# Optimization experiments

Hardware: AMD Instinct MI355X
Metric: run time of the kernel (lower is better)

## Reference

```python
import jax, jax.numpy as jnp
import numpy as np

N_NODES = 100000
N_EDGES = 1600000
IN_FEAT = 128
UNITS = 64


def setup_inputs() -> dict:
    key = jax.random.key(0)
    k1, k2, k3, k4, k5 = jax.random.split(key, 5)
    node_states = jax.random.normal(k1, (N_NODES, IN_FEAT), dtype=jnp.float32)
    # edges[:,0] is the destination/segment id; the original TF code's
    # repeat(bincount) normalization assumes edges sorted by edges[:,0].
    dst = jnp.sort(jax.random.randint(k2, (N_EDGES,), 0, N_NODES))
    src = jax.random.randint(k3, (N_EDGES,), 0, N_NODES)
    edges = jnp.stack([dst, src], axis=1).astype(jnp.int64)
    kernel = jax.random.normal(k4, (IN_FEAT, UNITS), dtype=jnp.float32) * 0.05
    kernel_attention = jax.random.normal(k5, (2 * UNITS, 1), dtype=jnp.float32) * 0.05
    return {"node_states": node_states, "edges": edges,
            "kernel": kernel, "kernel_attention": kernel_attention}


def reference(node_states, edges, kernel, kernel_attention):
    n_nodes = node_states.shape[0]
    dst = edges[:, 0]  # segment ids (aggregation target)
    src = edges[:, 1]  # neighbor being gathered

    h = node_states @ kernel                      # [N, U]
    h_dst = h[dst]                                # [E, U]
    h_src = h[src]                                # [E, U]
    # concat(h_dst, h_src) @ a  ==  h_dst @ a[:U] + h_src @ a[U:]
    u = kernel_attention.shape[0] // 2
    scores = (h_dst @ kernel_attention[:u] + h_src @ kernel_attention[u:])[:, 0]  # [E]
    scores = jax.nn.leaky_relu(scores, negative_slope=0.2)  # tf default alpha=0.2
    scores = jnp.exp(jnp.clip(scores, -2.0, 2.0))

    score_sum = jax.ops.segment_sum(scores, dst, num_segments=n_nodes)  # [N]
    attn = scores / score_sum[dst]                                      # [E]

    out = jax.ops.segment_sum(h_src * attn[:, None], dst, num_segments=n_nodes)  # [N, U]
    return out
```

## Files before the change

### kernel.cpp

```cpp
#include <hip/hip_runtime.h>
#include <hip/hip_bf16.h>

#define NN 100000
#define NE 1600000
#define NF 128
#define UU 64

typedef __attribute__((ext_vector_type(8))) short short8;
typedef __attribute__((ext_vector_type(4))) float f32x4;

static const size_t OFF_FLAG = 0;
static const size_t OFF_EW   = 256;
static const size_t OFF_H2   = OFF_EW  + (size_t)NE * 8;
static const size_t OFF_AD   = OFF_H2  + (size_t)NN * UU * 2;
static const size_t OFF_AS   = OFF_AD  + (size_t)NN * 4;
static const size_t OFF_ROW  = OFF_AS  + (size_t)NN * 4;
static const size_t OFF_WP   = OFF_ROW + (size_t)(NN + 1) * 4;

__device__ __forceinline__ unsigned short bfr(float v) {
    unsigned u = __float_as_uint(v);
    return (unsigned short)((u + 0x7FFFu + ((u >> 16) & 1u)) >> 16);
}

__global__ __launch_bounds__(256) void prep(const int* __restrict__ ew,
                                            const float* __restrict__ W,
                                            int* __restrict__ flag,
                                            unsigned short* __restrict__ Wp) {
    if (blockIdx.x == 0) {
        if (threadIdx.x == 0) {
            int a = ew[2 * 400000 + 1] | ew[2 * 800000 + 1] |
                    ew[2 * 1200000 + 1] | ew[2 * 1599999 + 1];
            *flag = (a == 0) ? 1 : 0;
        }
        return;
    }
    int i = (blockIdx.x - 1) * 256 + threadIdx.x;
    int j   = i & 7;
    int l15 = (i >> 3) & 15;
    int quad = (i >> 7) & 3;
    int kb  = (i >> 9) & 3;
    int nt  = i >> 11;
    Wp[i] = bfr(W[(size_t)(kb * 32 + quad * 8 + j) * UU + nt * 16 + l15]);
}

#define GEMM_BLOCKS   1563
#define ROWS_BLOCKS   391

__global__ __launch_bounds__(256) void mega(const float* __restrict__ X,
                                            const void* __restrict__ edges,
                                            const int* __restrict__ flag,
                                            const unsigned short* __restrict__ Wp,
                                            const float* __restrict__ ka,
                                            unsigned short* __restrict__ h2,
                                            float* __restrict__ a_dst,
                                            float* __restrict__ a_src,
                                            int* __restrict__ rows) {
    int bid = blockIdx.x;
    int tid = threadIdx.x;

    if (bid < GEMM_BLOCKS) {
        int wv = tid >> 6, lane = tid & 63;
        int quad = lane >> 4, l15 = lane & 15;
        int nb = bid * 64 + wv * 16;
        int row = nb + l15; if (row >= NN) row = NN - 1;
        const float* xr = X + (size_t)row * NF + quad * 8;

        short8 afrag[4];
#pragma unroll
        for (int kb = 0; kb < 4; kb++) {
            float4 p0 = *(const float4*)(xr + kb * 32);
            float4 p1 = *(const float4*)(xr + kb * 32 + 4);
            short8 a;
            a[0] = (short)bfr(p0.x); a[1] = (short)bfr(p0.y);
            a[2] = (short)bfr(p0.z); a[3] = (short)bfr(p0.w);
            a[4] = (short)bfr(p1.x); a[5] = (short)bfr(p1.y);
            a[6] = (short)bfr(p1.z); a[7] = (short)bfr(p1.w);
            afrag[kb] = a;
        }

        f32x4 acc[4] = {f32x4{0,0,0,0}, f32x4{0,0,0,0}, f32x4{0,0,0,0}, f32x4{0,0,0,0}};
        const short8* wpf = (const short8*)Wp;
#pragma unroll
        for (int nt = 0; nt < 4; nt++) {
#pragma unroll
            for (int kb = 0; kb < 4; kb++) {
                short8 b = wpf[((nt * 4 + kb) * 4 + quad) * 16 + l15];
                acc[nt] = __builtin_amdgcn_mfma_f32_16x16x32_bf16(afrag[kb], b, acc[nt], 0, 0, 0);
            }
        }

        float kad[4], kas[4];
#pragma unroll
        for (int nt = 0; nt < 4; nt++) {
            kad[nt] = ka[nt * 16 + l15];
            kas[nt] = ka[64 + nt * 16 + l15];
        }
#pragma unroll
        for (int r = 0; r < 4; r++) {
            int m = nb + quad * 4 + r;
            if (m < NN) {
#pragma unroll
                for (int nt = 0; nt < 4; nt++)
                    h2[(size_t)m * UU + nt * 16 + l15] = bfr(acc[nt][r]);
            }
            float pd = acc[0][r] * kad[0] + acc[1][r] * kad[1] + acc[2][r] * kad[2] + acc[3][r] * kad[3];
            float ps = acc[0][r] * kas[0] + acc[1][r] * kas[1] + acc[2][r] * kas[2] + acc[3][r] * kas[3];
            pd += __shfl_xor(pd, 1); pd += __shfl_xor(pd, 2);
            pd += __shfl_xor(pd, 4); pd += __shfl_xor(pd, 8);
            ps += __shfl_xor(ps, 1); ps += __shfl_xor(ps, 2);
            ps += __shfl_xor(ps, 4); ps += __shfl_xor(ps, 8);
            if (l15 == 0 && m < NN) { a_dst[m] = pd; a_src[m] = ps; }
        }
        return;
    }
    bid -= GEMM_BLOCKS;

    {
        int n = bid * 256 + tid;
        if (n > NN) return;
        if (n == NN) { rows[NN] = NE; return; }
        int fl = *flag;
        const int* ew = (const int*)edges;
        int lo = 0, hi = NE;
        while (lo < hi) {
            int mid = (lo + hi) >> 1;
            int d = fl ? ew[4 * (size_t)mid] : ew[2 * (size_t)mid];
            if (d < n) lo = mid + 1; else hi = mid;
        }
        rows[n] = lo;
    }
}

__device__ __forceinline__ float edge_score(float ad, float as) {
    float sc = ad + as;
    sc = sc > 0.f ? sc : 0.2f * sc;
    sc = fminf(fmaxf(sc, -2.f), 2.f);
    return __expf(sc);
}

__global__ __launch_bounds__(256) void wkern(const void* __restrict__ edges,
                                             const int* __restrict__ flag,
                                             const float* __restrict__ a_dst,
                                             const float* __restrict__ a_src,
                                             int2* __restrict__ ew8) {
    int fl = *flag;
    int tid = threadIdx.x;
    if (fl) {
        const int4* ev = (const int4*)edges;
#pragma unroll
        for (int t = 0; t < 4; t++) {
            int i = blockIdx.x * 1024 + t * 256 + tid;
            if (i < NE) {
                int4 v = ev[i];
                float w = edge_score(a_dst[v.x], a_src[v.z]);
                ew8[i] = make_int2(v.z, __float_as_int(w));
            }
        }
    } else {
        const int4* ev = (const int4*)edges;
#pragma unroll
        for (int t = 0; t < 2; t++) {
            int p = blockIdx.x * 512 + t * 256 + tid;
            if (p * 2 < NE) {
                int4 v = ev[p];
                float w0 = edge_score(a_dst[v.x], a_src[v.y]);
                float w1 = edge_score(a_dst[v.z], a_src[v.w]);
                int4 o = make_int4(v.y, __float_as_int(w0), v.w, __float_as_int(w1));
                *(int4*)(ew8 + p * 2) = o;
            }
        }
    }
}

__global__ __launch_bounds__(256) void aggregate(const int* __restrict__ rows,
                                                 const int2* __restrict__ ew8,
                                                 const unsigned short* __restrict__ h2,
                                                 float* __restrict__ out) {
    int gid = blockIdx.x * blockDim.x + threadIdx.x;
    int n = gid >> 6;
    int lane = gid & 63;
    if (n >= NN) return;
    int s = rows[n], e = rows[n + 1];
    int cnt = e - s;
    int g = lane >> 4, gl = lane & 15;
    const unsigned short* h2g = h2 + gl * 4;
    float4 acc = make_float4(0.f, 0.f, 0.f, 0.f);

#define GBATCH(C0, N)                                                            \
    {                                                                            \
        uint2 rr[4]; float sw[4]; int sjv[4];                                    \
        _Pragma("unroll")                                                        \
        for (int t = 0; t < (N); t++) {                                          \
            int j = (C0) + t * 4 + g;                                            \
            sjv[t] = __shfl(mysrc, j);                                           \
            sw[t]  = __shfl(myw, j);                                             \
        }                                                                        \
        _Pragma("unroll")                                                        \
        for (int t = 0; t < (N); t++)                                            \
            rr[t] = *(const uint2*)(h2g + (size_t)sjv[t] * UU);                  \
        _Pragma("unroll")                                                        \
        for (int t = 0; t < (N); t++) {                                          \
            acc.x += sw[t] * __uint_as_float(rr[t].x << 16);                     \
            acc.y += sw[t] * __uint_as_float(rr[t].x & 0xFFFF0000u);             \
            acc.z += sw[t] * __uint_as_float(rr[t].y << 16);                     \
            acc.w += sw[t] * __uint_as_float(rr[t].y & 0xFFFF0000u);             \
        }                                                                        \
    }

    float inv;
    if (cnt <= 64) {
        int idx = s + lane;
        int mysrc = 0; float myw = 0.f;
        if (idx < e) { int2 p = ew8[idx]; mysrc = p.x; myw = __int_as_float(p.y); }
        int c = 0;
        for (; c + 16 <= cnt; c += 16) GBATCH(c, 4);
        int rem = cnt - c;
        if (rem > 12)     GBATCH(c, 4)
        else if (rem > 8) GBATCH(c, 3)
        else if (rem > 4) GBATCH(c, 2)
        else if (rem > 0) GBATCH(c, 1);
        float t = myw;
#pragma unroll
        for (int off = 32; off; off >>= 1) t += __shfl_xor(t, off);
        inv = (cnt > 0) ? 1.f / t : 0.f;
    } else {
        float ssum = 0.f;
        for (int i = s + lane; i < e; i += 64) ssum += __int_as_float(ew8[i].y);
#pragma unroll
        for (int off = 32; off; off >>= 1) ssum += __shfl_xor(ssum, off);
        inv = 1.f / ssum;
        for (int c0 = s; c0 < e; c0 += 64) {
            int i = c0 + lane;
            int mysrc = 0; float myw = 0.f;
            if (i < e) { int2 p = ew8[i]; mysrc = p.x; myw = __int_as_float(p.y); }
            GBATCH(0, 4); GBATCH(16, 4); GBATCH(32, 4); GBATCH(48, 4);
        }
    }
#undef GBATCH

    acc.x += __shfl_xor(acc.x, 32); acc.y += __shfl_xor(acc.y, 32);
    acc.z += __shfl_xor(acc.z, 32); acc.w += __shfl_xor(acc.w, 32);
    acc.x += __shfl_xor(acc.x, 16); acc.y += __shfl_xor(acc.y, 16);
    acc.z += __shfl_xor(acc.z, 16); acc.w += __shfl_xor(acc.w, 16);
    if (lane < 16) {
        float4 o = make_float4(acc.x * inv, acc.y * inv, acc.z * inv, acc.w * inv);
        *(float4*)(out + (size_t)n * UU + gl * 4) = o;
    }
}

extern "C" void kernel_launch(void* const* d_in, const int* in_sizes, int n_in,
                              void* d_out, int out_size, void* d_ws, size_t ws_size,
                              hipStream_t stream) {
    const float* X  = (const float*)d_in[0];
    const void*  Ed = d_in[1];
    const float* W  = (const float*)d_in[2];
    const float* KA = (const float*)d_in[3];
    float* out = (float*)d_out;

    char* ws = (char*)d_ws;
    int*            flag  = (int*)(ws + OFF_FLAG);
    int2*           ew8   = (int2*)(ws + OFF_EW);
    unsigned short* h2    = (unsigned short*)(ws + OFF_H2);
    float*          a_dst = (float*)(ws + OFF_AD);
    float*          a_src = (float*)(ws + OFF_AS);
    int*            rows  = (int*)(ws + OFF_ROW);
    unsigned short* Wp    = (unsigned short*)(ws + OFF_WP);

    prep<<<33, 256, 0, stream>>>((const int*)Ed, W, flag, Wp);
    mega<<<GEMM_BLOCKS + ROWS_BLOCKS, 256, 0, stream>>>(
        X, Ed, flag, Wp, KA, h2, a_dst, a_src, rows);
    wkern<<<1563, 256, 0, stream>>>(Ed, flag, a_dst, a_src, ew8);
    aggregate<<<(NN * 64 + 255) / 256, 256, 0, stream>>>(rows, ew8, h2, out);
}
```

Measured before the change: 162.4 us.

## Fuse edge-score kernel into aggregation, one node per 16-lane group

Removes the separate wkern pass that wrote (src, weight) pairs to a workspace buffer. Attention scores are now computed inside the aggregation kernel straight from the edge array and a_src. Each wave now handles four nodes, one per 16-lane group, instead of one node per wave, which cuts idle lanes at an average degree of about 16. The cost is strided 8- or 16-byte reads of the int64 edge array, scattered a_src gathers inside the aggregate kernel, and more divergence when node degrees differ within a wave.

New measurement: 145.2 us. 10.6% less time.

```diff
diff --git a/kernel.cpp b/kernel.cpp
--- a/kernel.cpp
+++ b/kernel.cpp
@@ -10,8 +10,7 @@
 typedef __attribute__((ext_vector_type(4))) float f32x4;
 
 static const size_t OFF_FLAG = 0;
-static const size_t OFF_EW   = 256;
-static const size_t OFF_H2   = OFF_EW  + (size_t)NE * 8;
+static const size_t OFF_H2   = 256;
 static const size_t OFF_AD   = OFF_H2  + (size_t)NN * UU * 2;
 static const size_t OFF_AS   = OFF_AD  + (size_t)NN * 4;
 static const size_t OFF_ROW  = OFF_AS  + (size_t)NN * 4;
@@ -138,114 +137,101 @@
     return __expf(sc);
 }
 
-__global__ __launch_bounds__(256) void wkern(const void* __restrict__ edges,
-                                             const int* __restrict__ flag,
-                                             const float* __restrict__ a_dst,
-                                             const float* __restrict__ a_src,
-                                             int2* __restrict__ ew8) {
-    int fl = *flag;
-    int tid = threadIdx.x;
-    if (fl) {
-        const int4* ev = (const int4*)edges;
-#pragma unroll
-        for (int t = 0; t < 4; t++) {
-            int i = blockIdx.x * 1024 + t * 256 + tid;
-            if (i < NE) {
-                int4 v = ev[i];
-                float w = edge_score(a_dst[v.x], a_src[v.z]);
-                ew8[i] = make_int2(v.z, __float_as_int(w));
-            }
-        }
-    } else {
-        const int4* ev = (const int4*)edges;
-#pragma unroll
-        for (int t = 0; t < 2; t++) {
-            int p = blockIdx.x * 512 + t * 256 + tid;
-            if (p * 2 < NE) {
-                int4 v = ev[p];
-                float w0 = edge_score(a_dst[v.x], a_src[v.y]);
-                float w1 = edge_score(a_dst[v.z], a_src[v.w]);
-                int4 o = make_int4(v.y, __float_as_int(w0), v.w, __float_as_int(w1));
-                *(int4*)(ew8 + p * 2) = o;
-            }
-        }
-    }
-}
-
-__global__ __launch_bounds__(256) void aggregate(const int* __restrict__ rows,
-                                                 const int2* __restrict__ ew8,
+__global__ __launch_bounds__(256) void aggregate(const void* __restrict__ edges,
+                                                 const int* __restrict__ flag,
+                                                 const int* __restrict__ rows,
+                                                 const float* __restrict__ a_dst,
+                                                 const float* __restrict__ a_src,
                                                  const unsigned short* __restrict__ h2,
                                                  float* __restrict__ out) {
-    int gid = blockIdx.x * blockDim.x + threadIdx.x;
-    int n = gid >> 6;
-    int lane = gid & 63;
+    int tid = threadIdx.x;
+    int lane = tid & 63;
+    int g = lane >> 4, gl = lane & 15;
+    int n = blockIdx.x * 16 + (tid >> 6) * 4 + g;
     if (n >= NN) return;
     int s = rows[n], e = rows[n + 1];
     int cnt = e - s;
-    int g = lane >> 4, gl = lane & 15;
+    float ad = a_dst[n];
+    int fl = *flag;
+    const int* ew = (const int*)edges;
+    const int* sp = ew + (fl ? 2 : 1);
+    int lsh = fl ? 2 : 1;
     const unsigned short* h2g = h2 + gl * 4;
+    int gbase = g * 16;
     float4 acc = make_float4(0.f, 0.f, 0.f, 0.f);
-
-#define GBATCH(C0, N)                                                            \
-    {                                                                            \
-        uint2 rr[4]; float sw[4]; int sjv[4];                                    \
-        _Pragma("unroll")                                                        \
-        for (int t = 0; t < (N); t++) {                                          \
-            int j = (C0) + t * 4 + g;                                            \
-            sjv[t] = __shfl(mysrc, j);                                           \
-            sw[t]  = __shfl(myw, j);                                             \
-        }                                                                        \
-        _Pragma("unroll")                                                        \
-        for (int t = 0; t < (N); t++)                                            \
-            rr[t] = *(const uint2*)(h2g + (size_t)sjv[t] * UU);                  \
-        _Pragma("unroll")                                                        \
-        for (int t = 0; t < (N); t++) {                                          \
-            acc.x += sw[t] * __uint_as_float(rr[t].x << 16);                     \
-            acc.y += sw[t] * __uint_as_float(rr[t].x & 0xFFFF0000u);             \
-            acc.z += sw[t] * __uint_as_float(rr[t].y << 16);                     \
-            acc.w += sw[t] * __uint_as_float(rr[t].y & 0xFFFF0000u);             \
-        }                                                                        \
-    }
-
     float inv;
+
+#define BATCH(MS, MW, BOFF)                                                  \
+    {                                                                        \
+        uint2 rr[4]; float sw[4]; int sjv[4];                                \
+        _Pragma("unroll")                                                    \
+        for (int t = 0; t < 4; t++) {                                        \
+            sjv[t] = __shfl(MS, gbase + (BOFF) + t);                         \
+            sw[t]  = __shfl(MW, gbase + (BOFF) + t);                         \
+        }                                                                    \
+        _Pragma("unroll")                                                    \
+        for (int t = 0; t < 4; t++)                                          \
+            rr[t] = *(const uint2*)(h2g + (size_t)sjv[t] * UU);              \
+        _Pragma("unroll")                                                    \
+        for (int t = 0; t < 4; t++) {                                        \
+            acc.x += sw[t] * __uint_as_float(rr[t].x << 16);                 \
+            acc.y += sw[t] * __uint_as_float(rr[t].x & 0xFFFF0000u);         \
+            acc.z += sw[t] * __uint_as_float(rr[t].y << 16);                 \
+            acc.w += sw[t] * __uint_as_float(rr[t].y & 0xFFFF0000u);         \
+        }                                                                    \
+    }
+
     if (cnt <= 64) {
-        int idx = s + lane;
-        int mysrc = 0; float myw = 0.f;
-        if (idx < e) { int2 p = ew8[idx]; mysrc = p.x; myw = __int_as_float(p.y); }
-        int c = 0;
-        for (; c + 16 <= cnt; c += 16) GBATCH(c, 4);
-        int rem = cnt - c;
-        if (rem > 12)     GBATCH(c, 4)
-        else if (rem > 8) GBATCH(c, 3)
-        else if (rem > 4) GBATCH(c, 2)
-        else if (rem > 0) GBATCH(c, 1);
-        float t = myw;
-#pragma unroll
-        for (int off = 32; off; off >>= 1) t += __shfl_xor(t, off);
-        inv = (cnt > 0) ? 1.f / t : 0.f;
+        int msrc[4]; float mw[4];
+#pragma unroll
+        for (int k = 0; k < 4; k++) {
+            int c = k * 16 + gl;
+            int sj = 0; float w = 0.f;
+            if (c < cnt) {
+                sj = sp[(size_t)(s + c) << lsh];
+                w = edge_score(ad, a_src[sj]);
+            }
+            msrc[k] = sj; mw[k] = w;
+        }
+        float t0 = (mw[0] + mw[1]) + (mw[2] + mw[3]);
+        t0 += __shfl_xor(t0, 1); t0 += __shfl_xor(t0, 2);
+        t0 += __shfl_xor(t0, 4); t0 += __shfl_xor(t0, 8);
+        inv = (cnt > 0) ? 1.f / t0 : 0.f;
+#pragma unroll
+        for (int k = 0; k < 4; k++) {
+#pragma unroll
+            for (int b = 0; b < 4; b++) {
+                if (k * 16 + b * 4 < cnt) BATCH(msrc[k], mw[k], b * 4);
+            }
+        }
     } else {
-        float ssum = 0.f;
-        for (int i = s + lane; i < e; i += 64) ssum += __int_as_float(ew8[i].y);
-#pragma unroll
-        for (int off = 32; off; off >>= 1) ssum += __shfl_xor(ssum, off);
-        inv = 1.f / ssum;
-        for (int c0 = s; c0 < e; c0 += 64) {
-            int i = c0 + lane;
-            int mysrc = 0; float myw = 0.f;
-            if (i < e) { int2 p = ew8[i]; mysrc = p.x; myw = __int_as_float(p.y); }
-            GBATCH(0, 4); GBATCH(16, 4); GBATCH(32, 4); GBATCH(48, 4);
-        }
-    }
-#undef GBATCH
-
-    acc.x += __shfl_xor(acc.x, 32); acc.y += __shfl_xor(acc.y, 32);
-    acc.z += __shfl_xor(acc.z, 32); acc.w += __shfl_xor(acc.w, 32);
-    acc.x += __shfl_xor(acc.x, 16); acc.y += __shfl_xor(acc.y, 16);
-    acc.z += __shfl_xor(acc.z, 16); acc.w += __shfl_xor(acc.w, 16);
-    if (lane < 16) {
-        float4 o = make_float4(acc.x * inv, acc.y * inv, acc.z * inv, acc.w * inv);
-        *(float4*)(out + (size_t)n * UU + gl * 4) = o;
-    }
+        float t0 = 0.f;
+        for (int c = gl; c < cnt; c += 16) {
+            int sj = sp[(size_t)(s + c) << lsh];
+            t0 += edge_score(ad, a_src[sj]);
+        }
+        t0 += __shfl_xor(t0, 1); t0 += __shfl_xor(t0, 2);
+        t0 += __shfl_xor(t0, 4); t0 += __shfl_xor(t0, 8);
+        inv = 1.f / t0;
+        for (int c0 = 0; c0 < cnt; c0 += 16) {
+            int c = c0 + gl;
+            int sj = 0; float w = 0.f;
+            if (c < cnt) {
+                sj = sp[(size_t)(s + c) << lsh];
+                w = edge_score(ad, a_src[sj]);
+            }
+#pragma unroll
+            for (int b = 0; b < 4; b++) {
+                if (c0 + b * 4 < cnt) BATCH(sj, w, b * 4);
+            }
+        }
+    }
+#undef BATCH
+
+    float4 o;
+    o.x = acc.x * inv; o.y = acc.y * inv;
+    o.z = acc.z * inv; o.w = acc.w * inv;
+    *(float4*)(out + (size_t)n * UU + gl * 4) = o;
 }
 
 extern "C" void kernel_launch(void* const* d_in, const int* in_sizes, int n_in,
@@ -259,7 +245,6 @@
 
     char* ws = (char*)d_ws;
     int*            flag  = (int*)(ws + OFF_FLAG);
-    int2*           ew8   = (int2*)(ws + OFF_EW);
     unsigned short* h2    = (unsigned short*)(ws + OFF_H2);
     float*          a_dst = (float*)(ws + OFF_AD);
     float*          a_src = (float*)(ws + OFF_AS);
@@ -269,6 +254,5 @@
     prep<<<33, 256, 0, stream>>>((const int*)Ed, W, flag, Wp);
     mega<<<GEMM_BLOCKS + ROWS_BLOCKS, 256, 0, stream>>>(
         X, Ed, flag, Wp, KA, h2, a_dst, a_src, rows);
-    wkern<<<1563, 256, 0, stream>>>(Ed, flag, a_dst, a_src, ew8);
-    aggregate<<<(NN * 64 + 255) / 256, 256, 0, stream>>>(rows, ew8, h2, out);
-}
+    aggregate<<<NN / 16, 256, 0, stream>>>(Ed, flag, rows, a_dst, a_src, h2, out);
+}
```
